# Optimization experiments

Measured on AMD Instinct MI355X. Metric: run time of the kernel, lower is better.

Reference implementation:

```python
import jax, jax.numpy as jnp
import numpy as np

EPS = 1e-7  # K.epsilon()
ROUTINGS = 3
NUM_CAPSULE = 32
DIM_CAPSULE = 64

def _squash(x, axis=-1):
    # NOTE: this repo's 'squash' is just L2-ish normalization: x / sqrt(||x||^2 + eps)
    s2 = jnp.sum(jnp.square(x), axis=axis, keepdims=True)
    return x / jnp.sqrt(s2 + EPS)

def setup_inputs() -> dict:
    key = jax.random.key(0)
    k1, k2 = jax.random.split(key)
    u_vecs = jax.random.normal(k1, (32, 1024, 256), dtype=jnp.float32)
    # shared-weight capsule kernel: (1, input_dim_capsule, num_capsule*dim_capsule)
    W = jax.random.normal(k2, (1, 256, NUM_CAPSULE * DIM_CAPSULE), dtype=jnp.float32) * 0.05
    return {"u_vecs": u_vecs, "W": W}

def reference(u_vecs, W):
    B, N, D = u_vecs.shape
    # conv1d with width-1 kernel == matmul over feature dim
    u_hat = jnp.einsum('bnd,dm->bnm', u_vecs, W[0])          # [B, N, NC*DC]
    u_hat = u_hat.reshape(B, N, NUM_CAPSULE, DIM_CAPSULE)
    u_hat = jnp.transpose(u_hat, (0, 2, 1, 3))               # [B, NC, N, DC]

    b = jnp.zeros((B, NUM_CAPSULE, N), dtype=u_hat.dtype)    # routing logits
    v = None
    for i in range(ROUTINGS):
        c = jax.nn.softmax(b, axis=-1)                       # over input capsules
        s = jnp.einsum('bij,bijd->bid', c, u_hat)            # weighted sum
        v = _squash(s)                                       # [B, NC, DC]
        if i < ROUTINGS - 1:
            b = b + jnp.einsum('bid,bijd->bij', v, u_hat)    # agreement update
    return v
```

## Files before the change

### kernel.cpp

```cpp
#include <hip/hip_runtime.h>
#include <math.h>


typedef short v8s __attribute__((ext_vector_type(8)));
typedef short v4s __attribute__((ext_vector_type(4)));
typedef float v4f __attribute__((ext_vector_type(4)));

__device__ __forceinline__ unsigned short f2bf(float x) {
    unsigned u = __float_as_uint(x);
    u = u + 0x7fffu + ((u >> 16) & 1u);
    return (unsigned short)(u >> 16);
}
__device__ __forceinline__ float bf2f(unsigned short h) {
    return __uint_as_float(((unsigned)h) << 16);
}

__global__ __launch_bounds__(256) void k_init(const float* __restrict__ U,
                                              const float* __restrict__ W,
                                              float* __restrict__ t0p,
                                              float* __restrict__ WT,
                                              short* __restrict__ Ubf) {
    int bid = blockIdx.x, tid = threadIdx.x;
    if (bid < 512) {
        int b = bid >> 4, q = bid & 15;
        int row0 = (b << 10) + (q << 6);
        const float* Up = U + (row0 << 8) + tid;
        short* Ub = Ubf + (row0 << 8) + tid;
        float acc = 0.f;
        #pragma unroll 8
        for (int jl = 0; jl < 64; ++jl) {
            float x = Up[jl << 8];
            acc += x;
            Ub[jl << 8] = (short)f2bf(x);
        }
        t0p[(b << 12) + (q << 8) + tid] = acc * (1.0f / 1024.0f);
    } else {
        __shared__ float tile[64 * 65];
        int tix = bid - 512;
        int k0 = (tix >> 5) << 6, c0 = (tix & 31) << 6;
        int cc = tid & 63, g4 = tid >> 6;
        #pragma unroll
        for (int r = 0; r < 16; ++r) {
            int kk = (g4 << 4) + r;
            tile[kk * 65 + cc] = W[(k0 + kk) * 2048 + c0 + cc];
        }
        __syncthreads();
        int kk = tid & 63;
        #pragma unroll
        for (int r = 0; r < 16; ++r) {
            int c = (g4 << 4) + r;
            WT[(c0 + c) * 256 + k0 + kk] = tile[kk * 65 + c];
        }
    }
}

__global__ __launch_bounds__(256) void k_sv(const float* __restrict__ t0p,
                                            const float* __restrict__ tpart,
                                            const float* __restrict__ sefpart,
                                            const float* __restrict__ W,
                                            const float* __restrict__ WT,
                                            short* __restrict__ wbt_h,
                                            short* __restrict__ wbt_l,
                                            float* __restrict__ out,
                                            int mode, int writeOut) {
    __shared__ float t_lds[256];
    __shared__ float spart[256];
    __shared__ __align__(16) float v_lds[64];
    __shared__ __align__(16) v4f spartw[256];
    __shared__ float sefv_s;
    int bid = blockIdx.x, tid = threadIdx.x;
    int b = bid >> 5, iG = bid & 31;
    int bg = (b << 1) | (iG >> 4), il = iG & 15;

    float acc = 0.f;
    if (mode == 0) {
        const float* tb = t0p + (b << 12) + tid;
        #pragma unroll
        for (int q = 0; q < 16; ++q) acc += tb[q << 8];
        if (tid == 0) sefv_s = 1.0f;
    } else {
        const float* tb = tpart + (((bg << 4) + il) << 8) + tid;
        #pragma unroll
        for (int p = 0; p < 16; ++p) acc += tb[p << 18];
        if (tid == 0) {
            float s = 0.f;
            #pragma unroll
            for (int p = 0; p < 16; ++p) s += sefpart[(p << 10) + (bg << 4) + il];
            sefv_s = s;
        }
    }
    t_lds[tid] = acc;
    __syncthreads();

    int d = tid & 63, kq = tid >> 6;
    const float* Wc = W + ((kq << 6) * 2048) + (iG << 6) + d;
    float s = 0.f;
    #pragma unroll 4
    for (int kk = 0; kk < 64; ++kk)
        s += t_lds[(kq << 6) + kk] * Wc[kk * 2048];
    spart[tid] = s;
    __syncthreads();

    if (tid < 64) {
        float sv = spart[tid] + spart[tid + 64] + spart[tid + 128] + spart[tid + 192];
        float n2 = sv * sv;
        #pragma unroll
        for (int m = 1; m < 64; m <<= 1) n2 += __shfl_xor(n2, m, 64);
        float sf = sefv_s;
        float v = sv * rsqrtf(n2 + 1e-7f * sf * sf);
        v_lds[tid] = v;
        if (writeOut) out[(bid << 6) + tid] = v;
    }
    __syncthreads();
    if (writeOut) return;

    int k4 = tid & 63, dq = tid >> 6;
    const float4* WT4 = (const float4*)WT;
    v4f wp = {0.f, 0.f, 0.f, 0.f};
    #pragma unroll
    for (int dd = 0; dd < 16; ++dd) {
        float vv = v_lds[(dq << 4) + dd];
        float4 wt = WT4[((iG << 6) + (dq << 4) + dd) * 64 + k4];
        wp.x += vv * wt.x; wp.y += vv * wt.y; wp.z += vv * wt.z; wp.w += vv * wt.w;
    }
    spartw[(dq << 6) + k4] = wp;
    __syncthreads();
    if (tid < 64) {
        v4f w = spartw[tid] + spartw[64 + tid] + spartw[128 + tid] + spartw[192 + tid];
        float wv4[4] = {w.x, w.y, w.z, w.w};
        unsigned short wh[4], wl[4];
        #pragma unroll
        for (int e = 0; e < 4; ++e) {
            wh[e] = f2bf(wv4[e]);
            wl[e] = f2bf(wv4[e] - bf2f(wh[e]));
        }
        int base = (((bg << 4) + il) << 8) + (tid << 2);
        *(v4s*)&wbt_h[base] = (v4s){(short)wh[0], (short)wh[1], (short)wh[2], (short)wh[3]};
        *(v4s*)&wbt_l[base] = (v4s){(short)wl[0], (short)wl[1], (short)wl[2], (short)wl[3]};
    }
}

__global__ __launch_bounds__(1024, 8) void k_pass(const short* __restrict__ Ubf,
                                                  const short* __restrict__ wbt_h,
                                                  const short* __restrict__ wbt_l,
                                                  float* __restrict__ bmatg,
                                                  float* __restrict__ tpart_out,
                                                  float* __restrict__ sefpart_out,
                                                  int addold) {
    __shared__ short s_U[64 * 268];
    __shared__ short s_wh[16 * 264];
    __shared__ short s_wl[16 * 264];
    __shared__ short s_eh[16 * 72];
    __shared__ short s_el[16 * 72];
    __shared__ float s_red[16 * 320];
    __shared__ float s_sefp[16 * 16];

    const int tid = threadIdx.x, wv = tid >> 6, lane = tid & 63;
    const int quad = lane >> 4, nn = lane & 15;
    const int blk = blockIdx.x;
    const int b = blk & 31, pg = blk >> 5;
    const int p = pg >> 1, g2 = pg & 1;
    const int bg = (b << 1) | g2;
    const int rowbase = (b << 10) + (p << 6);

    const int mt2 = wv & 3, jq = wv >> 2;
    const int rr = (jq << 2) + quad;
    const int jloc = (mt2 << 4) + rr;
    const int ga = (((bg << 10) + (p << 6) + jloc) << 4) + nn;
    float bold = 0.f;
    if (addold) bold = bmatg[ga];

    if (tid < 512) {
        int row = tid >> 5, seg = tid & 31;
        int gidx = (((bg << 4) + row) << 8) + (seg << 3);
        *(v8s*)&s_wh[row * 264 + (seg << 3)] = *(const v8s*)(wbt_h + gidx);
        *(v8s*)&s_wl[row * 264 + (seg << 3)] = *(const v8s*)(wbt_l + gidx);
    }
    {
        const short* Ub = Ubf + (rowbase << 8);
        int col = tid & 31, row0 = tid >> 5;
        v8s u0 = *(const v8s*)(Ub + (row0 << 8) + (col << 3));
        v8s u1 = *(const v8s*)(Ub + ((row0 + 32) << 8) + (col << 3));
        *(v4s*)&s_U[row0 * 268 + (col << 3)]            = __builtin_shufflevector(u0, u0, 0, 1, 2, 3);
        *(v4s*)&s_U[row0 * 268 + (col << 3) + 4]        = __builtin_shufflevector(u0, u0, 4, 5, 6, 7);
        *(v4s*)&s_U[(row0 + 32) * 268 + (col << 3)]     = __builtin_shufflevector(u1, u1, 0, 1, 2, 3);
        *(v4s*)&s_U[(row0 + 32) * 268 + (col << 3) + 4] = __builtin_shufflevector(u1, u1, 4, 5, 6, 7);
    }
    __syncthreads();

    {
        const int mt = wv & 3, kq = wv >> 2;
        v4f dacc = {0.f, 0.f, 0.f, 0.f};
        #pragma unroll
        for (int c = 0; c < 2; ++c) {
            int kb = (kq << 6) + (c << 5) + (quad << 3);
            v8s a  = *(const v8s*)&s_U[((mt << 4) + nn) * 268 + kb];
            v8s bh = *(const v8s*)&s_wh[nn * 264 + kb];
            v8s bl = *(const v8s*)&s_wl[nn * 264 + kb];
            dacc = __builtin_amdgcn_mfma_f32_16x16x32_bf16(a, bh, dacc, 0, 0, 0);
            dacc = __builtin_amdgcn_mfma_f32_16x16x32_bf16(a, bl, dacc, 0, 0, 0);
        }
        #pragma unroll
        for (int r = 0; r < 4; ++r)
            s_red[wv * 320 + ((quad << 2) + r) * 20 + nn] = dacc[r];
    }
    __syncthreads();

    {
        float val = bold;
        #pragma unroll
        for (int kq = 0; kq < 4; ++kq)
            val += s_red[((kq << 2) + mt2) * 320 + rr * 20 + nn];
        if (!addold) bmatg[ga] = val;
        float e = __expf(val);
        unsigned short eh = f2bf(e);
        s_eh[nn * 72 + jloc] = (short)eh;
        s_el[nn * 72 + jloc] = (short)f2bf(e - bf2f(eh));
        float se = e;
        se += __shfl_xor(se, 16, 64);
        se += __shfl_xor(se, 32, 64);
        if (lane < 16) s_sefp[(wv << 4) + lane] = se;
    }
    __syncthreads();

    {
        v4f tacc = {0.f, 0.f, 0.f, 0.f};
        const int k0 = wv << 4;
        #pragma unroll
        for (int jc = 0; jc < 2; ++jc) {
            v8s aeh = *(const v8s*)&s_eh[nn * 72 + (jc << 5) + (quad << 3)];
            v8s ael = *(const v8s*)&s_el[nn * 72 + (jc << 5) + (quad << 3)];
            short bu[8];
            #pragma unroll
            for (int jj = 0; jj < 8; ++jj)
                bu[jj] = s_U[((jc << 5) + (quad << 3) + jj) * 268 + k0 + nn];
            v8s bf = (v8s){bu[0], bu[1], bu[2], bu[3], bu[4], bu[5], bu[6], bu[7]};
            tacc = __builtin_amdgcn_mfma_f32_16x16x32_bf16(aeh, bf, tacc, 0, 0, 0);
            tacc = __builtin_amdgcn_mfma_f32_16x16x32_bf16(ael, bf, tacc, 0, 0, 0);
        }
        #pragma unroll
        for (int r = 0; r < 4; ++r) {
            int i = (quad << 2) + r;
            tpart_out[(((((p << 6) + bg) << 4) + i) << 8) + k0 + nn] = tacc[r];
        }
    }
    if (tid < 16) {
        float ss = 0.f;
        #pragma unroll
        for (int w = 0; w < 16; ++w) ss += s_sefp[(w << 4) + tid];
        sefpart_out[(p << 10) + (bg << 4) + tid] = ss;
    }
}

extern "C" void kernel_launch(void* const* d_in, const int* in_sizes, int n_in,
                              void* d_out, int out_size, void* d_ws, size_t ws_size,
                              hipStream_t stream) {
    const float* U = (const float*)d_in[0];
    const float* W = (const float*)d_in[1];
    float* out = (float*)d_out;
    float* ws = (float*)d_ws;

    float* t0p   = ws;
    float* WT    = t0p + 131072;
    float* bmatg = WT + 524288;
    float* tp    = bmatg + 1048576;
    float* sef   = tp + 4194304;
    short* wbt_h = (short*)(sef + 16384);
    short* wbt_l = wbt_h + 262144;
    short* Ubf   = wbt_l + 262144;

    k_init<<<640, 256, 0, stream>>>(U, W, t0p, WT, Ubf);
    k_sv<<<1024, 256, 0, stream>>>(t0p, nullptr, nullptr, W, WT,
                                   wbt_h, wbt_l, out, 0, 0);
    k_pass<<<1024, 1024, 0, stream>>>(Ubf, wbt_h, wbt_l, bmatg, tp, sef, 0);
    k_sv<<<1024, 256, 0, stream>>>(t0p, tp, sef, W, WT,
                                   wbt_h, wbt_l, out, 1, 0);
    k_pass<<<1024, 1024, 0, stream>>>(Ubf, wbt_h, wbt_l, bmatg, tp, sef, 1);
    k_sv<<<1024, 256, 0, stream>>>(t0p, tp, sef, W, WT,
                                   wbt_h, wbt_l, out, 1, 1);
}
```

Before: 133.4 us.

## Fuse all routing stages into one persistent cooperative kernel with grid syncs

Replaces the chain of six kernel launches with a single cooperative kernel of 512 blocks that runs init, the s/v stages and the routing passes, separated by grid.sync. Each block keeps its bf16 U tile in LDS across both passes, so the Ubf global round trip goes away. Routing logits stay in registers instead of bmatg, and each block now handles both capsule groups for its rows. The fallback path keeps separate launches with the new 512-block pass kernel. The cost is grid-wide barriers, and the cooperative path is skipped when the stream is being captured.

```diff
diff --git a/kernel.cpp b/kernel.cpp
--- a/kernel.cpp
+++ b/kernel.cpp
@@ -1,5 +1,8 @@
 #include <hip/hip_runtime.h>
+#include <hip/hip_cooperative_groups.h>
 #include <math.h>
+
+namespace cg = cooperative_groups;
 
 
 typedef short v8s __attribute__((ext_vector_type(8)));
@@ -158,24 +161,22 @@
     const int tid = threadIdx.x, wv = tid >> 6, lane = tid & 63;
     const int quad = lane >> 4, nn = lane & 15;
     const int blk = blockIdx.x;
-    const int b = blk & 31, pg = blk >> 5;
-    const int p = pg >> 1, g2 = pg & 1;
-    const int bg = (b << 1) | g2;
+    const int b = blk & 31, p = blk >> 5;
     const int rowbase = (b << 10) + (p << 6);
 
     const int mt2 = wv & 3, jq = wv >> 2;
     const int rr = (jq << 2) + quad;
     const int jloc = (mt2 << 4) + rr;
-    const int ga = (((bg << 10) + (p << 6) + jloc) << 4) + nn;
-    float bold = 0.f;
-    if (addold) bold = bmatg[ga];
-
-    if (tid < 512) {
-        int row = tid >> 5, seg = tid & 31;
-        int gidx = (((bg << 4) + row) << 8) + (seg << 3);
-        *(v8s*)&s_wh[row * 264 + (seg << 3)] = *(const v8s*)(wbt_h + gidx);
-        *(v8s*)&s_wl[row * 264 + (seg << 3)] = *(const v8s*)(wbt_l + gidx);
-    }
+
+    float bold[2] = {0.f, 0.f};
+    if (addold) {
+        #pragma unroll
+        for (int g2 = 0; g2 < 2; ++g2) {
+            int bg = (b << 1) | g2;
+            bold[g2] = bmatg[(((bg << 10) + (p << 6) + jloc) << 4) + nn];
+        }
+    }
+
     {
         const short* Ub = Ubf + (rowbase << 8);
         int col = tid & 31, row0 = tid >> 5;
@@ -186,70 +187,359 @@
         *(v4s*)&s_U[(row0 + 32) * 268 + (col << 3)]     = __builtin_shufflevector(u1, u1, 0, 1, 2, 3);
         *(v4s*)&s_U[(row0 + 32) * 268 + (col << 3) + 4] = __builtin_shufflevector(u1, u1, 4, 5, 6, 7);
     }
-    __syncthreads();
+
+    #pragma unroll
+    for (int g2 = 0; g2 < 2; ++g2) {
+        const int bg = (b << 1) | g2;
+        if (tid < 512) {
+            int row = tid >> 5, seg = tid & 31;
+            int gidx = (((bg << 4) + row) << 8) + (seg << 3);
+            *(v8s*)&s_wh[row * 264 + (seg << 3)] = *(const v8s*)(wbt_h + gidx);
+            *(v8s*)&s_wl[row * 264 + (seg << 3)] = *(const v8s*)(wbt_l + gidx);
+        }
+        __syncthreads();
+
+        {
+            const int mt = wv & 3, kq = wv >> 2;
+            v4f dacc = {0.f, 0.f, 0.f, 0.f};
+            #pragma unroll
+            for (int c = 0; c < 2; ++c) {
+                int kb = (kq << 6) + (c << 5) + (quad << 3);
+                v8s a  = *(const v8s*)&s_U[((mt << 4) + nn) * 268 + kb];
+                v8s bh = *(const v8s*)&s_wh[nn * 264 + kb];
+                v8s bl = *(const v8s*)&s_wl[nn * 264 + kb];
+                dacc = __builtin_amdgcn_mfma_f32_16x16x32_bf16(a, bh, dacc, 0, 0, 0);
+                dacc = __builtin_amdgcn_mfma_f32_16x16x32_bf16(a, bl, dacc, 0, 0, 0);
+            }
+            #pragma unroll
+            for (int r = 0; r < 4; ++r)
+                s_red[wv * 320 + ((quad << 2) + r) * 20 + nn] = dacc[r];
+        }
+        __syncthreads();
+
+        {
+            float val = bold[g2];
+            #pragma unroll
+            for (int kq = 0; kq < 4; ++kq)
+                val += s_red[((kq << 2) + mt2) * 320 + rr * 20 + nn];
+            if (!addold)
+                bmatg[(((bg << 10) + (p << 6) + jloc) << 4) + nn] = val;
+            float e = __expf(val);
+            unsigned short eh = f2bf(e);
+            s_eh[nn * 72 + jloc] = (short)eh;
+            s_el[nn * 72 + jloc] = (short)f2bf(e - bf2f(eh));
+            float se = e;
+            se += __shfl_xor(se, 16, 64);
+            se += __shfl_xor(se, 32, 64);
+            if (lane < 16) s_sefp[(wv << 4) + lane] = se;
+        }
+        __syncthreads();
+
+        {
+            v4f tacc = {0.f, 0.f, 0.f, 0.f};
+            const int k0 = wv << 4;
+            #pragma unroll
+            for (int jc = 0; jc < 2; ++jc) {
+                v8s aeh = *(const v8s*)&s_eh[nn * 72 + (jc << 5) + (quad << 3)];
+                v8s ael = *(const v8s*)&s_el[nn * 72 + (jc << 5) + (quad << 3)];
+                short bu[8];
+                #pragma unroll
+                for (int jj = 0; jj < 8; ++jj)
+                    bu[jj] = s_U[((jc << 5) + (quad << 3) + jj) * 268 + k0 + nn];
+                v8s bf = (v8s){bu[0], bu[1], bu[2], bu[3], bu[4], bu[5], bu[6], bu[7]};
+                tacc = __builtin_amdgcn_mfma_f32_16x16x32_bf16(aeh, bf, tacc, 0, 0, 0);
+                tacc = __builtin_amdgcn_mfma_f32_16x16x32_bf16(ael, bf, tacc, 0, 0, 0);
+            }
+            #pragma unroll
+            for (int r = 0; r < 4; ++r) {
+                int i = (quad << 2) + r;
+                tpart_out[(((((p << 6) + bg) << 4) + i) << 8) + k0 + nn] = tacc[r];
+            }
+        }
+        if (tid < 16) {
+            float ss = 0.f;
+            #pragma unroll
+            for (int w = 0; w < 16; ++w) ss += s_sefp[(w << 4) + tid];
+            sefpart_out[(p << 10) + (bg << 4) + tid] = ss;
+        }
+    }
+}
+
+#define OFF_WH   34304
+#define OFF_WL   42752
+#define OFF_EH   51200
+#define OFF_EL   53504
+#define OFF_RED  55808
+#define OFF_SEFP 76288
+#define OFF_SV   34304
+#define SV_HALF  21504
+
+__device__ __forceinline__ void sv_stage(
+    char* smem, int bid, int tid,
+    const float* __restrict__ t0p, const float* __restrict__ tpart,
+    const float* __restrict__ sefpart, const float* __restrict__ W,
+    const float* __restrict__ WT, short* __restrict__ wbt_h,
+    short* __restrict__ wbt_l, float* __restrict__ out,
+    int mode, int writeOut)
+{
+    const int half = tid >> 9, stid = tid & 511;
+    const int u = (bid << 1) | half;
+    const int b = u >> 5, iG = u & 31;
+    const int bg = (b << 1) | (iG >> 4), il = iG & 15;
+    char* base = smem + OFF_SV + half * SV_HALF;
+    float* t_lds = (float*)base;
+    float* spart = (float*)(base + 1024);
+    float* v_lds = (float*)(base + 3072);
+    float* sefv  = (float*)(base + 3328);
+    v4f*  spartw = (v4f*)(base + 3344);
 
     {
-        const int mt = wv & 3, kq = wv >> 2;
-        v4f dacc = {0.f, 0.f, 0.f, 0.f};
-        #pragma unroll
-        for (int c = 0; c < 2; ++c) {
-            int kb = (kq << 6) + (c << 5) + (quad << 3);
-            v8s a  = *(const v8s*)&s_U[((mt << 4) + nn) * 268 + kb];
-            v8s bh = *(const v8s*)&s_wh[nn * 264 + kb];
-            v8s bl = *(const v8s*)&s_wl[nn * 264 + kb];
-            dacc = __builtin_amdgcn_mfma_f32_16x16x32_bf16(a, bh, dacc, 0, 0, 0);
-            dacc = __builtin_amdgcn_mfma_f32_16x16x32_bf16(a, bl, dacc, 0, 0, 0);
-        }
-        #pragma unroll
-        for (int r = 0; r < 4; ++r)
-            s_red[wv * 320 + ((quad << 2) + r) * 20 + nn] = dacc[r];
-    }
+        int col = stid & 255, h2 = stid >> 8;
+        float acc = 0.f;
+        if (mode == 0) {
+            const float* tb = t0p + (b << 12) + col;
+            #pragma unroll
+            for (int q = 0; q < 8; ++q) acc += tb[((h2 << 3) + q) << 8];
+        } else {
+            const float* tb = tpart + (((bg << 4) + il) << 8) + col;
+            #pragma unroll
+            for (int p = 0; p < 8; ++p) acc += tb[((h2 << 3) + p) << 18];
+        }
+        spart[(h2 << 8) + col] = acc;
+        if (stid == 0) {
+            if (mode == 0) sefv[0] = 1.0f;
+            else {
+                float s = 0.f;
+                #pragma unroll
+                for (int p = 0; p < 16; ++p)
+                    s += sefpart[(p << 10) + (bg << 4) + il];
+                sefv[0] = s;
+            }
+        }
+    }
+    __syncthreads();
+    if (stid < 256) t_lds[stid] = spart[stid] + spart[256 + stid];
     __syncthreads();
 
     {
-        float val = bold;
-        #pragma unroll
-        for (int kq = 0; kq < 4; ++kq)
-            val += s_red[((kq << 2) + mt2) * 320 + rr * 20 + nn];
-        if (!addold) bmatg[ga] = val;
-        float e = __expf(val);
-        unsigned short eh = f2bf(e);
-        s_eh[nn * 72 + jloc] = (short)eh;
-        s_el[nn * 72 + jloc] = (short)f2bf(e - bf2f(eh));
-        float se = e;
-        se += __shfl_xor(se, 16, 64);
-        se += __shfl_xor(se, 32, 64);
-        if (lane < 16) s_sefp[(wv << 4) + lane] = se;
-    }
-    __syncthreads();
+        int d = stid & 63, kq = stid >> 6;
+        const float* Wc = W + ((kq << 5) * 2048) + (iG << 6) + d;
+        float s = 0.f;
+        #pragma unroll 4
+        for (int kk = 0; kk < 32; ++kk)
+            s += t_lds[(kq << 5) + kk] * Wc[kk * 2048];
+        spart[(kq << 6) + d] = s;
+    }
+    __syncthreads();
+    if (stid < 64) {
+        float sv = 0.f;
+        #pragma unroll
+        for (int q = 0; q < 8; ++q) sv += spart[(q << 6) + stid];
+        float n2 = sv * sv;
+        #pragma unroll
+        for (int m = 1; m < 64; m <<= 1) n2 += __shfl_xor(n2, m, 64);
+        float sf = sefv[0];
+        float vv = sv * rsqrtf(n2 + 1e-7f * sf * sf);
+        v_lds[stid] = vv;
+        if (writeOut) out[(b << 11) + (iG << 6) + stid] = vv;
+    }
+    __syncthreads();
+    if (writeOut) return;
 
     {
-        v4f tacc = {0.f, 0.f, 0.f, 0.f};
-        const int k0 = wv << 4;
-        #pragma unroll
-        for (int jc = 0; jc < 2; ++jc) {
-            v8s aeh = *(const v8s*)&s_eh[nn * 72 + (jc << 5) + (quad << 3)];
-            v8s ael = *(const v8s*)&s_el[nn * 72 + (jc << 5) + (quad << 3)];
-            short bu[8];
-            #pragma unroll
-            for (int jj = 0; jj < 8; ++jj)
-                bu[jj] = s_U[((jc << 5) + (quad << 3) + jj) * 268 + k0 + nn];
-            v8s bf = (v8s){bu[0], bu[1], bu[2], bu[3], bu[4], bu[5], bu[6], bu[7]};
-            tacc = __builtin_amdgcn_mfma_f32_16x16x32_bf16(aeh, bf, tacc, 0, 0, 0);
-            tacc = __builtin_amdgcn_mfma_f32_16x16x32_bf16(ael, bf, tacc, 0, 0, 0);
-        }
-        #pragma unroll
-        for (int r = 0; r < 4; ++r) {
-            int i = (quad << 2) + r;
-            tpart_out[(((((p << 6) + bg) << 4) + i) << 8) + k0 + nn] = tacc[r];
-        }
-    }
-    if (tid < 16) {
-        float ss = 0.f;
-        #pragma unroll
-        for (int w = 0; w < 16; ++w) ss += s_sefp[(w << 4) + tid];
-        sefpart_out[(p << 10) + (bg << 4) + tid] = ss;
-    }
+        int k4 = stid & 63, dq = stid >> 6;
+        const float4* WT4 = (const float4*)WT;
+        v4f wp = {0.f, 0.f, 0.f, 0.f};
+        #pragma unroll
+        for (int dd = 0; dd < 8; ++dd) {
+            float vd = v_lds[(dq << 3) + dd];
+            float4 wt = WT4[(((iG << 6) + (dq << 3) + dd) << 6) + k4];
+            wp.x += vd * wt.x; wp.y += vd * wt.y;
+            wp.z += vd * wt.z; wp.w += vd * wt.w;
+        }
+        spartw[(dq << 6) + k4] = wp;
+    }
+    __syncthreads();
+    if (stid < 64) {
+        v4f w = spartw[stid];
+        #pragma unroll
+        for (int q = 1; q < 8; ++q) w += spartw[(q << 6) + stid];
+        float wv4[4] = {w.x, w.y, w.z, w.w};
+        unsigned short wh[4], wl[4];
+        #pragma unroll
+        for (int e = 0; e < 4; ++e) {
+            wh[e] = f2bf(wv4[e]);
+            wl[e] = f2bf(wv4[e] - bf2f(wh[e]));
+        }
+        int bs = (((bg << 4) + il) << 8) + (stid << 2);
+        *(v4s*)&wbt_h[bs] = (v4s){(short)wh[0], (short)wh[1], (short)wh[2], (short)wh[3]};
+        *(v4s*)&wbt_l[bs] = (v4s){(short)wl[0], (short)wl[1], (short)wl[2], (short)wl[3]};
+    }
+    __syncthreads();
+}
+
+__device__ __forceinline__ void pass_stage(
+    char* smem, int b, int pp, int tid,
+    const short* __restrict__ wbt_h, const short* __restrict__ wbt_l,
+    float* __restrict__ tpart, float* __restrict__ sefpart,
+    float* vlog, int pass)
+{
+    short* s_U    = (short*)smem;
+    short* s_wh   = (short*)(smem + OFF_WH);
+    short* s_wl   = (short*)(smem + OFF_WL);
+    short* s_eh   = (short*)(smem + OFF_EH);
+    short* s_el   = (short*)(smem + OFF_EL);
+    float* s_red  = (float*)(smem + OFF_RED);
+    float* s_sefp = (float*)(smem + OFF_SEFP);
+
+    const int wv = tid >> 6, lane = tid & 63;
+    const int quad = lane >> 4, nn = lane & 15;
+    const int mt2 = wv & 3, jq = wv >> 2;
+    const int rr = (jq << 2) + quad;
+    const int jloc = (mt2 << 4) + rr;
+
+    #pragma unroll
+    for (int g2 = 0; g2 < 2; ++g2) {
+        const int bg = (b << 1) | g2;
+        if (tid < 512) {
+            int row = tid >> 5, seg = tid & 31;
+            int gidx = (((bg << 4) + row) << 8) + (seg << 3);
+            *(v8s*)&s_wh[row * 264 + (seg << 3)] = *(const v8s*)(wbt_h + gidx);
+            *(v8s*)&s_wl[row * 264 + (seg << 3)] = *(const v8s*)(wbt_l + gidx);
+        }
+        __syncthreads();
+        {
+            const int mt = wv & 3, kq = wv >> 2;
+            v4f dacc = {0.f, 0.f, 0.f, 0.f};
+            #pragma unroll
+            for (int c = 0; c < 2; ++c) {
+                int kb = (kq << 6) + (c << 5) + (quad << 3);
+                v8s a  = *(const v8s*)&s_U[((mt << 4) + nn) * 268 + kb];
+                v8s bh = *(const v8s*)&s_wh[nn * 264 + kb];
+                v8s bl = *(const v8s*)&s_wl[nn * 264 + kb];
+                dacc = __builtin_amdgcn_mfma_f32_16x16x32_bf16(a, bh, dacc, 0, 0, 0);
+                dacc = __builtin_amdgcn_mfma_f32_16x16x32_bf16(a, bl, dacc, 0, 0, 0);
+            }
+            #pragma unroll
+            for (int r = 0; r < 4; ++r)
+                s_red[wv * 320 + ((quad << 2) + r) * 20 + nn] = dacc[r];
+        }
+        __syncthreads();
+        {
+            float val = pass ? vlog[g2] : 0.f;
+            #pragma unroll
+            for (int kq = 0; kq < 4; ++kq)
+                val += s_red[((kq << 2) + mt2) * 320 + rr * 20 + nn];
+            if (!pass) vlog[g2] = val;
+            float e = __expf(val);
+            unsigned short eh = f2bf(e);
+            s_eh[nn * 72 + jloc] = (short)eh;
+            s_el[nn * 72 + jloc] = (short)f2bf(e - bf2f(eh));
+            float se = e;
+            se += __shfl_xor(se, 16, 64);
+            se += __shfl_xor(se, 32, 64);
+            if (lane < 16) s_sefp[(wv << 4) + lane] = se;
+        }
+        __syncthreads();
+        {
+            v4f tacc = {0.f, 0.f, 0.f, 0.f};
+            const int k0 = wv << 4;
+            #pragma unroll
+            for (int jc = 0; jc < 2; ++jc) {
+                v8s aeh = *(const v8s*)&s_eh[nn * 72 + (jc << 5) + (quad << 3)];
+                v8s ael = *(const v8s*)&s_el[nn * 72 + (jc << 5) + (quad << 3)];
+                short bu[8];
+                #pragma unroll
+                for (int jj = 0; jj < 8; ++jj)
+                    bu[jj] = s_U[((jc << 5) + (quad << 3) + jj) * 268 + k0 + nn];
+                v8s bf = (v8s){bu[0], bu[1], bu[2], bu[3], bu[4], bu[5], bu[6], bu[7]};
+                tacc = __builtin_amdgcn_mfma_f32_16x16x32_bf16(aeh, bf, tacc, 0, 0, 0);
+                tacc = __builtin_amdgcn_mfma_f32_16x16x32_bf16(ael, bf, tacc, 0, 0, 0);
+            }
+            #pragma unroll
+            for (int r = 0; r < 4; ++r) {
+                int i = (quad << 2) + r;
+                tpart[(((((pp << 6) + bg) << 4) + i) << 8) + k0 + nn] = tacc[r];
+            }
+        }
+        if (tid < 16) {
+            float ss = 0.f;
+            #pragma unroll
+            for (int w = 0; w < 16; ++w) ss += s_sefp[(w << 4) + tid];
+            sefpart[(pp << 10) + (bg << 4) + tid] = ss;
+        }
+        __syncthreads();
+    }
+}
+
+__global__ __launch_bounds__(1024, 8) void k_all(
+    const float* __restrict__ U, const float* __restrict__ W,
+    float* __restrict__ out, float* __restrict__ t0p, float* __restrict__ WT,
+    float* __restrict__ tpart, float* __restrict__ sefpart,
+    short* __restrict__ wbt_h, short* __restrict__ wbt_l)
+{
+    __shared__ __align__(16) char smem[77312];
+    cg::grid_group grid = cg::this_grid();
+    const int tid = threadIdx.x, bid = blockIdx.x;
+    const int b = bid & 31, pp = bid >> 5;
+    float vlog[2];
+
+    {
+        short* s_U = (short*)smem;
+        v4f* cp4 = (v4f*)(smem + OFF_RED);
+        const float4* U4 = (const float4*)U;
+        const int rowbase = (b << 10) + (pp << 6);
+        int col = tid & 63, row0 = tid >> 6;
+        v4f psum = {0.f, 0.f, 0.f, 0.f};
+        #pragma unroll
+        for (int q = 0; q < 4; ++q) {
+            float4 g = U4[(rowbase + row0 + (q << 4)) * 64 + col];
+            psum.x += g.x; psum.y += g.y; psum.z += g.z; psum.w += g.w;
+            *(v4s*)&s_U[(row0 + (q << 4)) * 268 + (col << 2)] =
+                (v4s){(short)f2bf(g.x), (short)f2bf(g.y),
+                      (short)f2bf(g.z), (short)f2bf(g.w)};
+        }
+        cp4[(row0 << 6) + col] = psum;
+        __syncthreads();
+        if (tid < 256) {
+            const float* cp = (const float*)cp4;
+            float acc = 0.f;
+            #pragma unroll
+            for (int r0 = 0; r0 < 16; ++r0) acc += cp[(r0 << 8) + tid];
+            t0p[(b << 12) + (pp << 8) + tid] = acc * (1.0f / 1024.0f);
+        }
+        __syncthreads();
+        if (bid < 128) {
+            float* tile = (float*)(smem + OFF_RED);
+            int k0 = (bid >> 5) << 6, c0 = (bid & 31) << 6;
+            int cc = tid & 63, kk2 = tid >> 6;
+            #pragma unroll
+            for (int e = 0; e < 4; ++e) {
+                int kk = kk2 + (e << 4);
+                tile[kk * 65 + cc] = W[(k0 + kk) * 2048 + c0 + cc];
+            }
+            __syncthreads();
+            int kk = tid & 63, c2 = tid >> 6;
+            #pragma unroll
+            for (int e = 0; e < 4; ++e) {
+                int c = c2 + (e << 4);
+                WT[(c0 + c) * 256 + k0 + kk] = tile[kk * 65 + c];
+            }
+        }
+    }
+    grid.sync();
+    sv_stage((char*)smem, bid, tid, t0p, tpart, sefpart, W, WT,
+             wbt_h, wbt_l, out, 0, 0);
+    grid.sync();
+    pass_stage((char*)smem, b, pp, tid, wbt_h, wbt_l, tpart, sefpart, vlog, 0);
+    grid.sync();
+    sv_stage((char*)smem, bid, tid, t0p, tpart, sefpart, W, WT,
+             wbt_h, wbt_l, out, 1, 0);
+    grid.sync();
+    pass_stage((char*)smem, b, pp, tid, wbt_h, wbt_l, tpart, sefpart, vlog, 1);
+    grid.sync();
+    sv_stage((char*)smem, bid, tid, t0p, tpart, sefpart, W, WT,
+             wbt_h, wbt_l, out, 1, 1);
 }
 
 extern "C" void kernel_launch(void* const* d_in, const int* in_sizes, int n_in,
@@ -264,18 +554,35 @@
     float* WT    = t0p + 131072;
     float* bmatg = WT + 524288;
     float* tp    = bmatg + 1048576;
-    float* sef   = tp + 4194304;
-    short* wbt_h = (short*)(sef + 16384);
+    float* sefp  = tp + 4194304;
+    short* wbt_h = (short*)(sefp + 16384);
     short* wbt_l = wbt_h + 262144;
     short* Ubf   = wbt_l + 262144;
 
-    k_init<<<640, 256, 0, stream>>>(U, W, t0p, WT, Ubf);
-    k_sv<<<1024, 256, 0, stream>>>(t0p, nullptr, nullptr, W, WT,
-                                   wbt_h, wbt_l, out, 0, 0);
-    k_pass<<<1024, 1024, 0, stream>>>(Ubf, wbt_h, wbt_l, bmatg, tp, sef, 0);
-    k_sv<<<1024, 256, 0, stream>>>(t0p, tp, sef, W, WT,
-                                   wbt_h, wbt_l, out, 1, 0);
-    k_pass<<<1024, 1024, 0, stream>>>(Ubf, wbt_h, wbt_l, bmatg, tp, sef, 1);
-    k_sv<<<1024, 256, 0, stream>>>(t0p, tp, sef, W, WT,
-                                   wbt_h, wbt_l, out, 1, 1);
-}
+    hipError_t cerr = hipErrorUnknown;
+    hipStreamCaptureStatus cap = hipStreamCaptureStatusNone;
+    (void)hipStreamIsCapturing(stream, &cap);
+    if (cap == hipStreamCaptureStatusNone) {
+        int maxb = 0;
+        hipError_t oerr = hipOccupancyMaxActiveBlocksPerMultiprocessor(
+            &maxb, (const void*)k_all, 1024, 0);
+        if (oerr == hipSuccess && maxb >= 2) {
+            void* args[] = {(void*)&U, (void*)&W, (void*)&out, (void*)&t0p,
+                            (void*)&WT, (void*)&tp, (void*)&sefp,
+                            (void*)&wbt_h, (void*)&wbt_l};
+            cerr = hipLaunchCooperativeKernel((void*)k_all, dim3(512),
+                                              dim3(1024), args, 0, stream);
+        }
+    }
+    if (cerr != hipSuccess) {
+        k_init<<<640, 256, 0, stream>>>(U, W, t0p, WT, Ubf);
+        k_sv<<<1024, 256, 0, stream>>>(t0p, tp, sefp, W, WT,
+                                       wbt_h, wbt_l, out, 0, 0);
+        k_pass<<<512, 1024, 0, stream>>>(Ubf, wbt_h, wbt_l, bmatg, tp, sefp, 0);
+        k_sv<<<1024, 256, 0, stream>>>(t0p, tp, sefp, W, WT,
+                                       wbt_h, wbt_l, out, 1, 0);
+        k_pass<<<512, 1024, 0, stream>>>(Ubf, wbt_h, wbt_l, bmatg, tp, sefp, 1);
+        k_sv<<<1024, 256, 0, stream>>>(t0p, tp, sefp, W, WT,
+                                       wbt_h, wbt_l, out, 1, 1);
+    }
+}
```

Result: no change. 134.2 us (+0.6%).
